# Performance work log

Measured on AMD Instinct MI355X. Metric: run time of the kernel, lower is better.

The kernel has to match this reference:

```python
import jax, jax.numpy as jnp
import numpy as np

H = 16          # num_heads
LN_EPS = 1e-5   # torch LayerNorm default


def _ln(x, g, b):
    m = jnp.mean(x, axis=-1, keepdims=True)
    v = jnp.var(x, axis=-1, keepdims=True)
    return (x - m) * jax.lax.rsqrt(v + LN_EPS) * g + b


def _cross_attn(xq, xkv, wq, wk, wv, wp, bp):
    B, N, C = xq.shape
    d = C // H
    scale = d ** -0.5
    q = (xq @ wq).reshape(B, N, H, d).transpose(0, 2, 1, 3)   # bhnd
    k = (xkv @ wk).reshape(B, N, H, d).transpose(0, 2, 1, 3)
    v = (xkv @ wv).reshape(B, N, H, d).transpose(0, 2, 1, 3)
    attn = jax.nn.softmax(jnp.einsum('bhnd,bhmd->bhnm', q, k) * scale, axis=-1)
    out = jnp.einsum('bhnm,bhmd->bhnd', attn, v).transpose(0, 2, 1, 3).reshape(B, N, C)
    return out @ wp + bp


def setup_inputs() -> dict:
    key = jax.random.key(0)
    ks = jax.random.split(key, 16)
    B, N, C, Hid = 8, 1024, 1024, 4096
    s = 0.02
    inp = {
        'x_1': jax.random.normal(ks[0], (B, N, C), jnp.float32),
        'x_2': jax.random.normal(ks[1], (B, N, C), jnp.float32),
        'x_3': jax.random.normal(ks[2], (B, N, C), jnp.float32),
        'ln11_g': jnp.ones((C,), jnp.float32), 'ln11_b': jnp.zeros((C,), jnp.float32),
        'ln12_g': jnp.ones((C,), jnp.float32), 'ln12_b': jnp.zeros((C,), jnp.float32),
        'ln21_g': jnp.ones((C,), jnp.float32), 'ln21_b': jnp.zeros((C,), jnp.float32),
        'ln23_g': jnp.ones((C,), jnp.float32), 'ln23_b': jnp.zeros((C,), jnp.float32),
        'ln2_g': jnp.ones((C,), jnp.float32), 'ln2_b': jnp.zeros((C,), jnp.float32),
        'a1_wq': s * jax.random.normal(ks[3], (C, C), jnp.float32),
        'a1_wk': s * jax.random.normal(ks[4], (C, C), jnp.float32),
        'a1_wv': s * jax.random.normal(ks[5], (C, C), jnp.float32),
        'a1_wp': s * jax.random.normal(ks[6], (C, C), jnp.float32),
        'a1_bp': jnp.zeros((C,), jnp.float32),
        'a2_wq': s * jax.random.normal(ks[7], (C, C), jnp.float32),
        'a2_wk': s * jax.random.normal(ks[8], (C, C), jnp.float32),
        'a2_wv': s * jax.random.normal(ks[9], (C, C), jnp.float32),
        'a2_wp': s * jax.random.normal(ks[10], (C, C), jnp.float32),
        'a2_bp': jnp.zeros((C,), jnp.float32),
        'fc1_w': s * jax.random.normal(ks[11], (C, Hid), jnp.float32),
        'fc1_b': jnp.zeros((Hid,), jnp.float32),
        'fc2_w': s * jax.random.normal(ks[12], (Hid, C), jnp.float32),
        'fc2_b': jnp.zeros((C,), jnp.float32),
    }
    return inp


def reference(x_1, x_2, x_3,
              ln11_g, ln11_b, ln12_g, ln12_b, ln21_g, ln21_b, ln23_g, ln23_b,
              ln2_g, ln2_b,
              a1_wq, a1_wk, a1_wv, a1_wp, a1_bp,
              a2_wq, a2_wk, a2_wv, a2_wp, a2_bp,
              fc1_w, fc1_b, fc2_w, fc2_b):
    # dual cross-attention branches + residual (drop_path/dropout are identity at p=0)
    br1 = _cross_attn(_ln(x_1, ln11_g, ln11_b), _ln(x_2, ln12_g, ln12_b),
                      a1_wq, a1_wk, a1_wv, a1_wp, a1_bp)
    br2 = _cross_attn(_ln(x_1, ln21_g, ln21_b), _ln(x_3, ln23_g, ln23_b),
                      a2_wq, a2_wk, a2_wv, a2_wp, a2_bp)
    x = x_1 + br1 + br2
    # MLP block
    h = jax.nn.gelu(_ln(x, ln2_g, ln2_b) @ fc1_w + fc1_b, approximate=False)
    x = x + (h @ fc2_w + fc2_b)
    return x
```

## Files before the change

### kernel.cpp

```cpp
#include <hip/hip_runtime.h>
#include <hip/hip_bf16.h>
#include <cstdint>

typedef unsigned short u16;
typedef __bf16 v8bf __attribute__((ext_vector_type(8)));
typedef short v4s __attribute__((ext_vector_type(4)));
typedef float v4f __attribute__((ext_vector_type(4)));

__device__ __forceinline__ u16 f2bf(float f) {
  union { float f; uint32_t u; } v; v.f = f;
  return (u16)((v.u + 0x7fffu + ((v.u >> 16) & 1u)) >> 16);
}
__device__ __forceinline__ float bf2f(u16 u) {
  union { uint32_t u; float f; } v; v.u = ((uint32_t)u) << 16; return v.f;
}
__device__ __forceinline__ float ex2(float x) {
  float r; asm("v_exp_f32 %0, %1" : "=v"(r) : "v"(x)); return r;
}

#define GLL16(gsrc, ldst) \
  __builtin_amdgcn_global_load_lds((__attribute__((address_space(1))) void*)(gsrc), \
      (__attribute__((address_space(3))) void*)(ldst), 16, 0, 0)

#define TILE_MAP(blk, bm, bn) \
  int bm = ((blk) & 7) * 8 + (((blk) >> 3) & 7); \
  int bn = (blk) >> 6;

__device__ __forceinline__ void gemm_core(
    const u16* __restrict__ A, const u16* __restrict__ Bt, int K,
    char* la, char* lb, int bm, int bn, int tid, v4f acc[4][4])
{
  int wv = tid >> 6, lane = tid & 63, quad = lane >> 4, lc = lane & 15;
  int wm = wv & 1, wn = wv >> 1;
  for (int kt = 0; kt < K; kt += 64) {
    __syncthreads();
    #pragma unroll
    for (int c0 = 0; c0 < 4; ++c0) {
      int chunk = wv*4 + c0;
      int off = chunk*1024 + lane*16;
      int row = off >> 7;
      int sc  = (off >> 4) & 7;
      int lg  = sc ^ (row & 7);
      GLL16(A  + (size_t)(bm*128 + row) * K + kt + lg*8, la + chunk*1024);
      GLL16(Bt + (size_t)(bn*128 + row) * K + kt + lg*8, lb + chunk*1024);
    }
    __syncthreads();
    #pragma unroll
    for (int kc = 0; kc < 2; ++kc) {
      v8bf af[4], bfr[4];
      #pragma unroll
      for (int r = 0; r < 4; ++r) {
        int row = wm*64 + r*16 + lc;
        int sc = (kc*4 + quad) ^ (row & 7);
        af[r] = *(const v8bf*)(la + row*128 + sc*16);
      }
      #pragma unroll
      for (int c = 0; c < 4; ++c) {
        int row = wn*64 + c*16 + lc;
        int sc = (kc*4 + quad) ^ (row & 7);
        bfr[c] = *(const v8bf*)(lb + row*128 + sc*16);
      }
      #pragma unroll
      for (int r = 0; r < 4; ++r)
        #pragma unroll
        for (int c = 0; c < 4; ++c)
          acc[r][c] = __builtin_amdgcn_mfma_f32_16x16x32_bf16(af[r], bfr[c], acc[r][c], 0, 0, 0);
    }
  }
}

__device__ __forceinline__ void lds_put16(char* lds_, int row, int col, u16 v) {
  *(u16*)(lds_ + row*256 + (((col >> 4) ^ (row & 7)) << 5) + (col & 15)*2) = v;
}
__device__ __forceinline__ void sweep128(const char* lds_, u16* gout, size_t ldc, int tid) {
  int sub = tid >> 4, j = tid & 15;
  #pragma unroll
  for (int p = 0; p < 8; ++p) {
    int row = p*16 + sub;
    uint4 d = *(const uint4*)(lds_ + row*256 + ((((j >> 1) ^ (row & 7)) << 5) + ((j & 1) << 4)));
    *(uint4*)(gout + (size_t)row*ldc + j*8) = d;
  }
}

struct TDesc { const float* W; u16* WT; int K, N, tstart; };

__device__ __forceinline__ void do_transpose(const TDesc& D, int loc, int tid, float* sh) {
  const float* W = D.W;
  u16* WT = D.WT;
  int K = D.K, N = D.N;
  int tiles_n = N >> 5;
  int bn = loc % tiles_n, bk = loc / tiles_n;
  int tx = tid & 31, ty = tid >> 5;
  #pragma unroll
  for (int j = 0; j < 4; ++j)
    sh[(ty + j*8)*33 + tx] = W[(size_t)(bk*32 + ty + j*8) * N + bn*32 + tx];
  __syncthreads();
  #pragma unroll
  for (int j = 0; j < 4; ++j)
    WT[(size_t)(bn*32 + ty + j*8) * K + bk*32 + tx] = f2bf(sh[tx*33 + ty + j*8]);
}

__device__ __forceinline__ void ln_f32_row(const float* x, const float* g, const float* b,
                                           u16* out, int row, int tid, float* red)
{
  float4 v = ((const float4*)(x + (size_t)row * 1024))[tid];
  float s = v.x + v.y + v.z + v.w;
  float ss = v.x*v.x + v.y*v.y + v.z*v.z + v.w*v.w;
  for (int d = 1; d < 64; d <<= 1) { s += __shfl_xor(s, d); ss += __shfl_xor(ss, d); }
  int wv = tid >> 6, lane = tid & 63;
  if (lane == 0) { red[wv] = s; red[4 + wv] = ss; }
  __syncthreads();
  s  = red[0] + red[1] + red[2] + red[3];
  ss = red[4] + red[5] + red[6] + red[7];
  float mean = s * (1.f/1024.f);
  float var  = ss * (1.f/1024.f) - mean*mean;
  float rs = rsqrtf(var + 1e-5f);
  float4 gv = ((const float4*)g)[tid];
  float4 bv = ((const float4*)b)[tid];
  ushort4 o;
  o.x = f2bf((v.x-mean)*rs*gv.x + bv.x);
  o.y = f2bf((v.y-mean)*rs*gv.y + bv.y);
  o.z = f2bf((v.z-mean)*rs*gv.z + bv.z);
  o.w = f2bf((v.w-mean)*rs*gv.w + bv.w);
  ((ushort4*)out)[(size_t)row*256 + tid] = o;
}

__device__ __forceinline__ void ln_f32_row2(const float* x,
    const float* g1, const float* b1, const float* g2, const float* b2,
    u16* o1, u16* o2, int row, int tid, float* red)
{
  float4 v = ((const float4*)(x + (size_t)row * 1024))[tid];
  float s = v.x + v.y + v.z + v.w;
  float ss = v.x*v.x + v.y*v.y + v.z*v.z + v.w*v.w;
  for (int d = 1; d < 64; d <<= 1) { s += __shfl_xor(s, d); ss += __shfl_xor(ss, d); }
  int wv = tid >> 6, lane = tid & 63;
  if (lane == 0) { red[wv] = s; red[4 + wv] = ss; }
  __syncthreads();
  s  = red[0] + red[1] + red[2] + red[3];
  ss = red[4] + red[5] + red[6] + red[7];
  float mean = s * (1.f/1024.f);
  float var  = ss * (1.f/1024.f) - mean*mean;
  float rs = rsqrtf(var + 1e-5f);
  float4 xn;
  xn.x = (v.x-mean)*rs; xn.y = (v.y-mean)*rs; xn.z = (v.z-mean)*rs; xn.w = (v.w-mean)*rs;
  {
    float4 gv = ((const float4*)g1)[tid];
    float4 bv = ((const float4*)b1)[tid];
    ushort4 o;
    o.x = f2bf(xn.x*gv.x + bv.x); o.y = f2bf(xn.y*gv.y + bv.y);
    o.z = f2bf(xn.z*gv.z + bv.z); o.w = f2bf(xn.w*gv.w + bv.w);
    ((ushort4*)o1)[(size_t)row*256 + tid] = o;
  }
  {
    float4 gv = ((const float4*)g2)[tid];
    float4 bv = ((const float4*)b2)[tid];
    ushort4 o;
    o.x = f2bf(xn.x*gv.x + bv.x); o.y = f2bf(xn.y*gv.y + bv.y);
    o.z = f2bf(xn.z*gv.z + bv.z); o.w = f2bf(xn.w*gv.w + bv.w);
    ((ushort4*)o2)[(size_t)row*256 + tid] = o;
  }
}

struct PrepAll {
  TDesc d[10];
  const float *x1, *g11, *b11, *g21, *b21;
  const float *x2, *g12, *b12;
  const float *x3, *g23, *b23;
  u16 *xq1, *xq2, *xkv1, *xkv2;
  int ts;
};
__global__ __launch_bounds__(256) void prep_all_kernel(PrepAll P)
{
  __shared__ float sh[32*33];
  int tid = threadIdx.x;
  int bi = blockIdx.x;
  if (bi < P.ts) {
    int idx = 0;
    #pragma unroll
    for (int i = 1; i < 10; ++i) if (bi >= P.d[i].tstart) idx = i;
    do_transpose(P.d[idx], bi - P.d[idx].tstart, tid, sh);
  } else {
    int lid = bi - P.ts;
    if (lid < 8192)
      ln_f32_row2(P.x1, P.g11, P.b11, P.g21, P.b21, P.xq1, P.xq2, lid, tid, sh);
    else if (lid < 16384)
      ln_f32_row(P.x2, P.g12, P.b12, P.xkv1, lid - 8192, tid, sh);
    else
      ln_f32_row(P.x3, P.g23, P.b23, P.xkv2, lid - 16384, tid, sh);
  }
}

__global__ __launch_bounds__(256) void ln_bf16_kernel(
    const u16* __restrict__ x, const float* __restrict__ g, const float* __restrict__ bt,
    u16* __restrict__ out)
{
  int row = blockIdx.x, tid = threadIdx.x;
  ushort4 xr = ((const ushort4*)x)[(size_t)row*256 + tid];
  float4 v;
  v.x = bf2f(xr.x); v.y = bf2f(xr.y); v.z = bf2f(xr.z); v.w = bf2f(xr.w);
  float s = v.x + v.y + v.z + v.w;
  float ss = v.x*v.x + v.y*v.y + v.z*v.z + v.w*v.w;
  for (int d = 1; d < 64; d <<= 1) { s += __shfl_xor(s, d); ss += __shfl_xor(ss, d); }
  __shared__ float red[8];
  int wv = tid >> 6, lane = tid & 63;
  if (lane == 0) { red[wv] = s; red[4 + wv] = ss; }
  __syncthreads();
  s  = red[0] + red[1] + red[2] + red[3];
  ss = red[4] + red[5] + red[6] + red[7];
  float mean = s * (1.f/1024.f);
  float var  = ss * (1.f/1024.f) - mean*mean;
  float rs = rsqrtf(var + 1e-5f);
  float4 gv = ((const float4*)g)[tid];
  float4 bv = ((const float4*)bt)[tid];
  ushort4 o;
  o.x = f2bf((v.x-mean)*rs*gv.x + bv.x);
  o.y = f2bf((v.y-mean)*rs*gv.y + bv.y);
  o.z = f2bf((v.z-mean)*rs*gv.z + bv.z);
  o.w = f2bf((v.w-mean)*rs*gv.w + bv.w);
  ((ushort4*)out)[(size_t)row*256 + tid] = o;
}

struct QkvArgs { const u16* A[3]; const u16* Bt[3]; u16* C[3]; };

__device__ __forceinline__ void qkv_body(const QkvArgs& P, int blk, int tid, char* lds_)
{
  int sub = blk >> 9;
  int local = blk & 511;
  TILE_MAP(local, bm, bn)
  int wv = tid >> 6, lane = tid & 63, quad = lane >> 4, lc = lane & 15;
  int wm = wv & 1, wn = wv >> 1;
  v4f acc[4][4] = {};
  gemm_core(P.A[sub], P.Bt[sub], 1024, lds_, lds_ + 16384, bm, bn, tid, acc);
  u16* Cout = P.C[sub];
  __syncthreads();
  if (sub == 2) {
    #pragma unroll
    for (int r = 0; r < 4; ++r) {
      int rl = wm*64 + r*16 + quad*4;
      #pragma unroll
      for (int c = 0; c < 4; ++c) {
        int cl = wn*64 + c*16 + lc;
        #pragma unroll
        for (int i = 0; i < 4; ++i)
          lds_put16(lds_, cl, rl + i, f2bf(acc[r][c][i]));
      }
    }
    __syncthreads();
    sweep128(lds_, Cout + (size_t)(bn*128) * 8192 + bm*128, 8192, tid);
  } else {
    #pragma unroll
    for (int r = 0; r < 4; ++r) {
      int lrow = wm*64 + r*16 + quad*4;
      #pragma unroll
      for (int c = 0; c < 4; ++c) {
        int lcol = wn*64 + c*16 + lc;
        #pragma unroll
        for (int i = 0; i < 4; ++i)
          lds_put16(lds_, lrow + i, lcol, f2bf(acc[r][c][i]));
      }
    }
    __syncthreads();
    sweep128(lds_, Cout + (size_t)(bm*128) * 1024 + bn*128, 1024, tid);
  }
}

__global__ __launch_bounds__(256, 4) void gemm_qkv(QkvArgs P)
{
  __shared__ __align__(16) char lds_[32768];
  qkv_body(P, blockIdx.x, threadIdx.x, lds_);
}

__device__ __forceinline__ void attn_body(
    const u16* __restrict__ Q, const u16* __restrict__ K, const u16* __restrict__ VT,
    u16* __restrict__ O, int bid, int tid, char* lds_)
{
  int qt = bid & 15, h = (bid >> 4) & 15, b = bid >> 8;
  int wv = tid >> 6, lane = tid & 63, quad = lane >> 4, lc = lane & 15;
  char* kt_l = lds_;
  char* vt_l = lds_ + 16384;
  const float cl2 = 0.18033688f;

  v8bf qf[2];
  {
    int qrow = qt*64 + wv*16 + lc;
    const u16* qp = Q + ((size_t)(b*1024 + qrow) * 1024 + h*64 + quad*8);
    qf[0] = *(const v8bf*)qp;
    qf[1] = *(const v8bf*)(qp + 32);
  }

  float m_i = -1e30f, l_i = 0.f;
  v4f oacc[4] = {};

  for (int it = 0; it < 8; ++it) {
    int kvb = it * 128;
    __syncthreads();
    #pragma unroll
    for (int c0 = 0; c0 < 4; ++c0) {
      int ch = wv*4 + c0;
      int off = ch*1024 + lane*16;
      {
        int row = off >> 7, sc = (off >> 4) & 7, lg = sc ^ (row & 7);
        GLL16(K + (size_t)(b*1024 + kvb + row) * 1024 + h*64 + lg*8, kt_l + ch*1024);
      }
      {
        int row = off >> 8, sc = (off >> 4) & 15, lg = sc ^ (row & 15);
        GLL16(VT + (size_t)(h*64 + row) * 8192 + b*1024 + kvb + lg*8, vt_l + ch*1024);
      }
    }
    __syncthreads();

    v4f s[8] = {};
    #pragma unroll
    for (int ct = 0; ct < 8; ++ct) {
      int row = ct*16 + lc;
      #pragma unroll
      for (int kc = 0; kc < 2; ++kc) {
        int sc = (kc*4 + quad) ^ (row & 7);
        v8bf kf = *(const v8bf*)(kt_l + row*128 + sc*16);
        s[ct] = __builtin_amdgcn_mfma_f32_16x16x32_bf16(kf, qf[kc], s[ct], 0, 0, 0);
      }
    }

    #pragma unroll
    for (int ct = 0; ct < 8; ++ct)
      #pragma unroll
      for (int i = 0; i < 4; ++i) s[ct][i] *= cl2;
    float mx = m_i;
    #pragma unroll
    for (int ct = 0; ct < 8; ++ct)
      #pragma unroll
      for (int i = 0; i < 4; ++i) mx = fmaxf(mx, s[ct][i]);
    mx = fmaxf(mx, __shfl_xor(mx, 16));
    mx = fmaxf(mx, __shfl_xor(mx, 32));
    float alpha = ex2(m_i - mx);
    float rs = 0.f;
    #pragma unroll
    for (int ct = 0; ct < 8; ++ct)
      #pragma unroll
      for (int i = 0; i < 4; ++i) {
        float p = ex2(s[ct][i] - mx);
        s[ct][i] = p;
        rs += p;
      }
    rs += __shfl_xor(rs, 16);
    rs += __shfl_xor(rs, 32);
    l_i = l_i * alpha + rs;
    m_i = mx;
    #pragma unroll
    for (int dt = 0; dt < 4; ++dt)
      #pragma unroll
      for (int i = 0; i < 4; ++i) oacc[dt][i] *= alpha;

    #pragma unroll
    for (int ct = 0; ct < 8; ++ct) {
      v4s pfrag;
      #pragma unroll
      for (int i = 0; i < 4; ++i) pfrag[i] = (short)f2bf(s[ct][i]);
      int lg = ct*2 + (quad >> 1);
      int ho = (quad & 1) * 8;
      #pragma unroll
      for (int dt = 0; dt < 4; ++dt) {
        int rowd = dt*16 + lc;
        int sc = lg ^ (rowd & 15);
        v4s vfrag = *(const v4s*)(vt_l + rowd*256 + sc*16 + ho);
        oacc[dt] = __builtin_amdgcn_mfma_f32_16x16x16bf16_1k(vfrag, pfrag, oacc[dt], 0, 0, 0);
      }
    }
  }

  __syncthreads();
  {
    char* base = kt_l + wv*2048;
    float inv = 1.f / l_i;
    #pragma unroll
    for (int dt = 0; dt < 4; ++dt) {
      ushort4 o;
      o.x = f2bf(oacc[dt][0]*inv); o.y = f2bf(oacc[dt][1]*inv);
      o.z = f2bf(oacc[dt][2]*inv); o.w = f2bf(oacc[dt][3]*inv);
      int lg = dt*2 + (quad >> 1);
      int sc = lg ^ (lc & 7);
      *(ushort4*)(base + lc*128 + sc*16 + (quad & 1)*8) = o;
    }
  }
  __syncthreads();
  {
    char* base = kt_l + wv*2048;
    #pragma unroll
    for (int rep = 0; rep < 2; ++rep) {
      int qr = rep*8 + (lane >> 3);
      int ch = lane & 7;
      int sc = ch ^ (qr & 7);
      uint4 d = *(const uint4*)(base + qr*128 + sc*16);
      *(uint4*)(O + (size_t)(b*1024 + qt*64 + wv*16 + qr) * 1024 + h*64 + ch*8) = d;
    }
  }
}

__global__ __launch_bounds__(256, 4) void attn_kernel(
    const u16* __restrict__ Q, const u16* __restrict__ K, const u16* __restrict__ VT,
    u16* __restrict__ O)
{
  __shared__ __align__(16) char lds_[32768];
  attn_body(Q, K, VT, O, blockIdx.x, threadIdx.x, lds_);
}

__global__ __launch_bounds__(256, 4) void attn_qkv_kernel(
    const u16* __restrict__ Q, const u16* __restrict__ K, const u16* __restrict__ VT,
    u16* __restrict__ O, QkvArgs G)
{
  __shared__ __align__(16) char lds_[32768];
  int tid = threadIdx.x;
  if ((int)blockIdx.x < 2048)
    attn_body(Q, K, VT, O, blockIdx.x, tid, lds_);
  else
    qkv_body(G, blockIdx.x - 2048, tid, lds_);
}

__global__ __launch_bounds__(256, 4) void attn_proj_kernel(
    const u16* __restrict__ Q, const u16* __restrict__ K, const u16* __restrict__ VT,
    u16* __restrict__ O,
    const u16* __restrict__ GA, const u16* __restrict__ GBt,
    const float* __restrict__ Gbias, u16* __restrict__ GC)
{
  __shared__ __align__(16) char lds_[32768];
  int tid = threadIdx.x;
  if ((int)blockIdx.x < 2048) {
    attn_body(Q, K, VT, O, blockIdx.x, tid, lds_);
  } else {
    int local = blockIdx.x - 2048;
    TILE_MAP(local, bm, bn)
    int wv = tid >> 6, lane = tid & 63, quad = lane >> 4, lc = lane & 15;
    int wm = wv & 1, wn = wv >> 1;
    v4f acc[4][4] = {};
    gemm_core(GA, GBt, 1024, lds_, lds_ + 16384, bm, bn, tid, acc);
    __syncthreads();
    #pragma unroll
    for (int r = 0; r < 4; ++r) {
      int lrow = wm*64 + r*16 + quad*4;
      #pragma unroll
      for (int c = 0; c < 4; ++c) {
        int lcol = wn*64 + c*16 + lc;
        float bv = Gbias[bn*128 + lcol];
        #pragma unroll
        for (int i = 0; i < 4; ++i)
          lds_put16(lds_, lrow + i, lcol, f2bf(acc[r][c][i] + bv));
      }
    }
    __syncthreads();
    sweep128(lds_, GC + (size_t)(bm*128) * 1024 + bn*128, 1024, tid);
  }
}

__global__ __launch_bounds__(256, 4) void gemm_projadd(
    const u16* __restrict__ A, const u16* __restrict__ Bt,
    const float* __restrict__ bias, const float* __restrict__ x1,
    const u16* __restrict__ o1b, u16* __restrict__ xsum)
{
  TILE_MAP((int)blockIdx.x, bm, bn)
  int tid = threadIdx.x, wv = tid >> 6, lane = tid & 63, quad = lane >> 4, lc = lane & 15;
  int wm = wv & 1, wn = wv >> 1;
  __shared__ __align__(16) char lds_[32768];
  v4f acc[4][4] = {};
  gemm_core(A, Bt, 1024, lds_, lds_ + 16384, bm, bn, tid, acc);
  __syncthreads();
  #pragma unroll
  for (int r = 0; r < 4; ++r) {
    int lrow = wm*64 + r*16 + quad*4;
    int grow = bm*128 + lrow;
    #pragma unroll
    for (int c = 0; c < 4; ++c) {
      int lcol = wn*64 + c*16 + lc;
      int gcol = bn*128 + lcol;
      float bv = bias[gcol];
      #pragma unroll
      for (int i = 0; i < 4; ++i) {
        size_t idx = (size_t)(grow + i) * 1024 + gcol;
        lds_put16(lds_, lrow + i, lcol, f2bf(acc[r][c][i] + bv + x1[idx] + bf2f(o1b[idx])));
      }
    }
  }
  __syncthreads();
  sweep128(lds_, xsum + (size_t)(bm*128) * 1024 + bn*128, 1024, tid);
}

__global__ __launch_bounds__(256, 2) void gemm_fc1(
    const u16* __restrict__ A, const u16* __restrict__ Bt,
    const float* __restrict__ bias, u16* __restrict__ C)
{
  int bm = blockIdx.x >> 5, bn = blockIdx.x & 31;
  int tid = threadIdx.x, wv = tid >> 6, lane = tid & 63, quad = lane >> 4, lc = lane & 15;
  int wm = wv & 1, wn = wv >> 1;
  __shared__ __align__(16) char lds_[32768];
  v4f acc[4][4] = {};
  gemm_core(A, Bt, 1024, lds_, lds_ + 16384, bm, bn, tid, acc);
  __syncthreads();
  #pragma unroll
  for (int r = 0; r < 4; ++r) {
    int lrow = wm*64 + r*16 + quad*4;
    #pragma unroll
    for (int c = 0; c < 4; ++c) {
      int lcol = wn*64 + c*16 + lc;
      float bv = bias[bn*128 + lcol];
      #pragma unroll
      for (int i = 0; i < 4; ++i) {
        float v = acc[r][c][i] + bv;
        float u2 = fminf(2.3023840f * (v + 0.044715f * v * v * v), 115.f);
        float t = ex2(u2);
        lds_put16(lds_, lrow + i, lcol, f2bf(v * t / (t + 1.f)));
      }
    }
  }
  __syncthreads();
  sweep128(lds_, C + (size_t)(bm*128) * 4096 + bn*128, 4096, tid);
}

__global__ __launch_bounds__(256, 3) void gemm_fc2(
    const u16* __restrict__ A, const u16* __restrict__ Bt,
    const float* __restrict__ bias, const u16* __restrict__ r1,
    float* __restrict__ C)
{
  TILE_MAP((int)blockIdx.x, bm, bn)
  int tid = threadIdx.x, wv = tid >> 6, lane = tid & 63, quad = lane >> 4, lc = lane & 15;
  int wm = wv & 1, wn = wv >> 1;
  __shared__ __align__(16) char lds_[32768];
  v4f acc[4][4] = {};
  gemm_core(A, Bt, 4096, lds_, lds_ + 16384, bm, bn, tid, acc);
  #pragma unroll
  for (int r = 0; r < 4; ++r) {
    int grow = bm*128 + wm*64 + r*16 + quad*4;
    #pragma unroll
    for (int c = 0; c < 4; ++c) {
      int gcol = bn*128 + wn*64 + c*16 + lc;
      float bv = bias[gcol];
      #pragma unroll
      for (int i = 0; i < 4; ++i) {
        size_t idx = (size_t)(grow + i) * 1024 + gcol;
        C[idx] = acc[r][c][i] + bv + bf2f(r1[idx]);
      }
    }
  }
}

extern "C" void kernel_launch(void* const* d_in, const int* in_sizes, int n_in,
                              void* d_out, int out_size, void* d_ws, size_t ws_size,
                              hipStream_t stream)
{
  const float* x1    = (const float*)d_in[0];
  const float* x2    = (const float*)d_in[1];
  const float* x3    = (const float*)d_in[2];
  const float* ln11g = (const float*)d_in[3];
  const float* ln11b = (const float*)d_in[4];
  const float* ln12g = (const float*)d_in[5];
  const float* ln12b = (const float*)d_in[6];
  const float* ln21g = (const float*)d_in[7];
  const float* ln21b = (const float*)d_in[8];
  const float* ln23g = (const float*)d_in[9];
  const float* ln23b = (const float*)d_in[10];
  const float* ln2g  = (const float*)d_in[11];
  const float* ln2b  = (const float*)d_in[12];
  const float* a1wq  = (const float*)d_in[13];
  const float* a1wk  = (const float*)d_in[14];
  const float* a1wv  = (const float*)d_in[15];
  const float* a1wp  = (const float*)d_in[16];
  const float* a1bp  = (const float*)d_in[17];
  const float* a2wq  = (const float*)d_in[18];
  const float* a2wk  = (const float*)d_in[19];
  const float* a2wv  = (const float*)d_in[20];
  const float* a2wp  = (const float*)d_in[21];
  const float* a2bp  = (const float*)d_in[22];
  const float* fc1w  = (const float*)d_in[23];
  const float* fc1b  = (const float*)d_in[24];
  const float* fc2w  = (const float*)d_in[25];
  const float* fc2b  = (const float*)d_in[26];

  char* ws = (char*)d_ws;
  const size_t MB = (size_t)1 << 20;
  u16* wtq1 = (u16*)(ws + 0*MB);  u16* wtk1 = (u16*)(ws + 2*MB);
  u16* wtv1 = (u16*)(ws + 4*MB);  u16* wtp1 = (u16*)(ws + 6*MB);
  u16* wtq2 = (u16*)(ws + 8*MB);  u16* wtk2 = (u16*)(ws + 10*MB);
  u16* wtv2 = (u16*)(ws + 12*MB); u16* wtp2 = (u16*)(ws + 14*MB);
  u16* wtf1 = (u16*)(ws + 16*MB); u16* wtf2 = (u16*)(ws + 24*MB);
  u16* xq1  = (u16*)(ws + 32*MB); u16* xkv1 = (u16*)(ws + 48*MB);
  u16* xq2  = (u16*)(ws + 64*MB); u16* xkv2 = (u16*)(ws + 80*MB);
  u16* Qb   = (u16*)(ws + 96*MB); u16* Kb   = (u16*)(ws + 112*MB);
  u16* VTb  = (u16*)(ws + 128*MB);
  u16* O1   = (u16*)(ws + 32*MB);
  u16* o1b  = (u16*)(ws + 64*MB);
  u16* xsum = (u16*)(ws + 112*MB);
  u16* ln2o = (u16*)(ws + 32*MB);
  u16* hbuf = (u16*)(ws + 48*MB);

  bool fused23 = (ws_size >= (size_t)176 * MB);
  u16 *Q2, *K2, *VT2, *O2;
  if (fused23) {
    Q2  = (u16*)(ws + 48*MB);
    K2  = (u16*)(ws + 144*MB);
    VT2 = (u16*)(ws + 160*MB);
    O2  = (u16*)(ws + 96*MB);
  } else {
    Q2 = Qb; K2 = Kb; VT2 = VTb;
    O2  = (u16*)(ws + 48*MB);
  }

  dim3 blk(256);

  PrepAll pa;
  {
    const float* Ws[10]  = {a1wq, a1wk, a1wv, a1wp, a2wq, a2wk, a2wv, a2wp, fc1w, fc2w};
    u16* WTs[10]         = {wtq1, wtk1, wtv1, wtp1, wtq2, wtk2, wtv2, wtp2, wtf1, wtf2};
    int Kd[10] = {1024,1024,1024,1024,1024,1024,1024,1024,1024,4096};
    int Nd[10] = {1024,1024,1024,1024,1024,1024,1024,1024,4096,1024};
    int ts = 0;
    for (int i = 0; i < 10; ++i) {
      pa.d[i] = {Ws[i], WTs[i], Kd[i], Nd[i], ts};
      ts += (Kd[i]/32) * (Nd[i]/32);
    }
    pa.ts = ts;
  }
  pa.x1 = x1; pa.g11 = ln11g; pa.b11 = ln11b; pa.g21 = ln21g; pa.b21 = ln21b;
  pa.x2 = x2; pa.g12 = ln12g; pa.b12 = ln12b;
  pa.x3 = x3; pa.g23 = ln23g; pa.b23 = ln23b;
  pa.xq1 = xq1; pa.xq2 = xq2; pa.xkv1 = xkv1; pa.xkv2 = xkv2;
  prep_all_kernel<<<pa.ts + 24576, blk, 0, stream>>>(pa);

  QkvArgs g1;
  g1.A[0]=xq1;  g1.Bt[0]=wtq1; g1.C[0]=Qb;
  g1.A[1]=xkv1; g1.Bt[1]=wtk1; g1.C[1]=Kb;
  g1.A[2]=xkv1; g1.Bt[2]=wtv1; g1.C[2]=VTb;
  gemm_qkv<<<1536, blk, 0, stream>>>(g1);

  QkvArgs g2;
  g2.A[0]=xq2;  g2.Bt[0]=wtq2; g2.C[0]=Q2;
  g2.A[1]=xkv2; g2.Bt[1]=wtk2; g2.C[1]=K2;
  g2.A[2]=xkv2; g2.Bt[2]=wtv2; g2.C[2]=VT2;
  if (fused23) {
    attn_qkv_kernel<<<2048 + 1536, blk, 0, stream>>>(Qb, Kb, VTb, O1, g2);
  } else {
    attn_kernel<<<2048, blk, 0, stream>>>(Qb, Kb, VTb, O1);
    gemm_qkv<<<1536, blk, 0, stream>>>(g2);
  }

  attn_proj_kernel<<<2048 + 512, blk, 0, stream>>>(Q2, K2, VT2, O2, O1, wtp1, a1bp, o1b);

  gemm_projadd<<<512, blk, 0, stream>>>(O2, wtp2, a2bp, x1, o1b, xsum);

  ln_bf16_kernel<<<8192, blk, 0, stream>>>(xsum, ln2g, ln2b, ln2o);

  gemm_fc1<<<2048, blk, 0, stream>>>(ln2o, wtf1, fc1b, hbuf);

  gemm_fc2<<<512, blk, 0, stream>>>(hbuf, wtf2, fc2b, xsum, (float*)d_out);
}
```

Before: 693.2 us.

## Fold softmax scale into Q, add lazy rescaling, pack conversions, tune occupancy

The softmax scale (log2e/sqrt(d)) is now folded into the Q projection epilogue, so the attention loop no longer multiplies every score. Online softmax skips rescaling the output accumulator when the new block max stays within a threshold of the running max, and P is converted to bf16 with packed hardware converts. Other changes: the V^T epilogue writes 4-element vectors with a new LDS swizzle, the LN kernel handles four rows per block, and the attention kernels raise launch-bound occupancy to 5. The lazy rescale lets exponents reach up to 2^8 before renormalising, and the higher occupancy target may force register spills.

```diff
diff --git a/kernel.cpp b/kernel.cpp
--- a/kernel.cpp
+++ b/kernel.cpp
@@ -25,6 +25,8 @@
 #define TILE_MAP(blk, bm, bn) \
   int bm = ((blk) & 7) * 8 + (((blk) >> 3) & 7); \
   int bn = (blk) >> 6;
+
+#define QSCALE 0.18033688f
 
 __device__ __forceinline__ void gemm_core(
     const u16* __restrict__ A, const u16* __restrict__ Bt, int K,
@@ -194,30 +196,35 @@
     const u16* __restrict__ x, const float* __restrict__ g, const float* __restrict__ bt,
     u16* __restrict__ out)
 {
-  int row = blockIdx.x, tid = threadIdx.x;
-  ushort4 xr = ((const ushort4*)x)[(size_t)row*256 + tid];
-  float4 v;
-  v.x = bf2f(xr.x); v.y = bf2f(xr.y); v.z = bf2f(xr.z); v.w = bf2f(xr.w);
-  float s = v.x + v.y + v.z + v.w;
-  float ss = v.x*v.x + v.y*v.y + v.z*v.z + v.w*v.w;
-  for (int d = 1; d < 64; d <<= 1) { s += __shfl_xor(s, d); ss += __shfl_xor(ss, d); }
+  int tid = threadIdx.x;
   __shared__ float red[8];
-  int wv = tid >> 6, lane = tid & 63;
-  if (lane == 0) { red[wv] = s; red[4 + wv] = ss; }
-  __syncthreads();
-  s  = red[0] + red[1] + red[2] + red[3];
-  ss = red[4] + red[5] + red[6] + red[7];
-  float mean = s * (1.f/1024.f);
-  float var  = ss * (1.f/1024.f) - mean*mean;
-  float rs = rsqrtf(var + 1e-5f);
   float4 gv = ((const float4*)g)[tid];
   float4 bv = ((const float4*)bt)[tid];
-  ushort4 o;
-  o.x = f2bf((v.x-mean)*rs*gv.x + bv.x);
-  o.y = f2bf((v.y-mean)*rs*gv.y + bv.y);
-  o.z = f2bf((v.z-mean)*rs*gv.z + bv.z);
-  o.w = f2bf((v.w-mean)*rs*gv.w + bv.w);
-  ((ushort4*)out)[(size_t)row*256 + tid] = o;
+  #pragma unroll
+  for (int rr = 0; rr < 4; ++rr) {
+    int row = blockIdx.x*4 + rr;
+    ushort4 xr = ((const ushort4*)x)[(size_t)row*256 + tid];
+    float4 v;
+    v.x = bf2f(xr.x); v.y = bf2f(xr.y); v.z = bf2f(xr.z); v.w = bf2f(xr.w);
+    float s = v.x + v.y + v.z + v.w;
+    float ss = v.x*v.x + v.y*v.y + v.z*v.z + v.w*v.w;
+    for (int d = 1; d < 64; d <<= 1) { s += __shfl_xor(s, d); ss += __shfl_xor(ss, d); }
+    int wv = tid >> 6, lane = tid & 63;
+    if (lane == 0) { red[wv] = s; red[4 + wv] = ss; }
+    __syncthreads();
+    s  = red[0] + red[1] + red[2] + red[3];
+    ss = red[4] + red[5] + red[6] + red[7];
+    float mean = s * (1.f/1024.f);
+    float var  = ss * (1.f/1024.f) - mean*mean;
+    float rs = rsqrtf(var + 1e-5f);
+    ushort4 o;
+    o.x = f2bf((v.x-mean)*rs*gv.x + bv.x);
+    o.y = f2bf((v.y-mean)*rs*gv.y + bv.y);
+    o.z = f2bf((v.z-mean)*rs*gv.z + bv.z);
+    o.w = f2bf((v.w-mean)*rs*gv.w + bv.w);
+    ((ushort4*)out)[(size_t)row*256 + tid] = o;
+    __syncthreads();
+  }
 }
 
 struct QkvArgs { const u16* A[3]; const u16* Bt[3]; u16* C[3]; };
@@ -240,14 +247,17 @@
       #pragma unroll
       for (int c = 0; c < 4; ++c) {
         int cl = wn*64 + c*16 + lc;
+        v4s o;
         #pragma unroll
-        for (int i = 0; i < 4; ++i)
-          lds_put16(lds_, cl, rl + i, f2bf(acc[r][c][i]));
+        for (int i = 0; i < 4; ++i) o[i] = (short)f2bf(acc[r][c][i]);
+        int chunk = ((rl >> 4) ^ (cl & 7)) << 5;
+        *(v4s*)(lds_ + cl*256 + chunk + (rl & 15)*2) = o;
       }
     }
     __syncthreads();
     sweep128(lds_, Cout + (size_t)(bn*128) * 8192 + bm*128, 8192, tid);
   } else {
+    float scl = (sub == 0) ? QSCALE : 1.f;
     #pragma unroll
     for (int r = 0; r < 4; ++r) {
       int lrow = wm*64 + r*16 + quad*4;
@@ -256,7 +266,7 @@
         int lcol = wn*64 + c*16 + lc;
         #pragma unroll
         for (int i = 0; i < 4; ++i)
-          lds_put16(lds_, lrow + i, lcol, f2bf(acc[r][c][i]));
+          lds_put16(lds_, lrow + i, lcol, f2bf(acc[r][c][i] * scl));
       }
     }
     __syncthreads();
@@ -278,7 +288,6 @@
   int wv = tid >> 6, lane = tid & 63, quad = lane >> 4, lc = lane & 15;
   char* kt_l = lds_;
   char* vt_l = lds_ + 16384;
-  const float cl2 = 0.18033688f;
 
   v8bf qf[2];
   {
@@ -321,18 +330,17 @@
       }
     }
 
+    float pmax = s[0][0];
     #pragma unroll
     for (int ct = 0; ct < 8; ++ct)
       #pragma unroll
-      for (int i = 0; i < 4; ++i) s[ct][i] *= cl2;
-    float mx = m_i;
-    #pragma unroll
-    for (int ct = 0; ct < 8; ++ct)
-      #pragma unroll
-      for (int i = 0; i < 4; ++i) mx = fmaxf(mx, s[ct][i]);
-    mx = fmaxf(mx, __shfl_xor(mx, 16));
-    mx = fmaxf(mx, __shfl_xor(mx, 32));
-    float alpha = ex2(m_i - mx);
+      for (int i = 0; i < 4; ++i) pmax = fmaxf(pmax, s[ct][i]);
+    pmax = fmaxf(pmax, __shfl_xor(pmax, 16));
+    pmax = fmaxf(pmax, __shfl_xor(pmax, 32));
+
+    bool stable = __all(pmax <= m_i + 8.f);
+    float mx = stable ? m_i : fmaxf(m_i, pmax);
+
     float rs = 0.f;
     #pragma unroll
     for (int ct = 0; ct < 8; ++ct)
@@ -344,18 +352,24 @@
       }
     rs += __shfl_xor(rs, 16);
     rs += __shfl_xor(rs, 32);
-    l_i = l_i * alpha + rs;
-    m_i = mx;
-    #pragma unroll
-    for (int dt = 0; dt < 4; ++dt)
-      #pragma unroll
-      for (int i = 0; i < 4; ++i) oacc[dt][i] *= alpha;
+    if (stable) {
+      l_i += rs;
+    } else {
+      float alpha = ex2(m_i - mx);
+      l_i = l_i * alpha + rs;
+      #pragma unroll
+      for (int dt = 0; dt < 4; ++dt)
+        #pragma unroll
+        for (int i = 0; i < 4; ++i) oacc[dt][i] *= alpha;
+      m_i = mx;
+    }
 
     #pragma unroll
     for (int ct = 0; ct < 8; ++ct) {
-      v4s pfrag;
-      #pragma unroll
-      for (int i = 0; i < 4; ++i) pfrag[i] = (short)f2bf(s[ct][i]);
+      union { uint32_t u[2]; v4s p; } pk;
+      asm("v_cvt_pk_bf16_f32 %0, %1, %2" : "=v"(pk.u[0]) : "v"(s[ct][0]), "v"(s[ct][1]));
+      asm("v_cvt_pk_bf16_f32 %0, %1, %2" : "=v"(pk.u[1]) : "v"(s[ct][2]), "v"(s[ct][3]));
+      v4s pfrag = pk.p;
       int lg = ct*2 + (quad >> 1);
       int ho = (quad & 1) * 8;
       #pragma unroll
@@ -396,7 +410,7 @@
   }
 }
 
-__global__ __launch_bounds__(256, 4) void attn_kernel(
+__global__ __launch_bounds__(256, 5) void attn_kernel(
     const u16* __restrict__ Q, const u16* __restrict__ K, const u16* __restrict__ VT,
     u16* __restrict__ O)
 {
@@ -404,7 +418,7 @@
   attn_body(Q, K, VT, O, blockIdx.x, threadIdx.x, lds_);
 }
 
-__global__ __launch_bounds__(256, 4) void attn_qkv_kernel(
+__global__ __launch_bounds__(256, 5) void attn_qkv_kernel(
     const u16* __restrict__ Q, const u16* __restrict__ K, const u16* __restrict__ VT,
     u16* __restrict__ O, QkvArgs G)
 {
@@ -416,7 +430,7 @@
     qkv_body(G, blockIdx.x - 2048, tid, lds_);
 }
 
-__global__ __launch_bounds__(256, 4) void attn_proj_kernel(
+__global__ __launch_bounds__(256, 5) void attn_proj_kernel(
     const u16* __restrict__ Q, const u16* __restrict__ K, const u16* __restrict__ VT,
     u16* __restrict__ O,
     const u16* __restrict__ GA, const u16* __restrict__ GBt,
@@ -644,7 +658,7 @@
 
   gemm_projadd<<<512, blk, 0, stream>>>(O2, wtp2, a2bp, x1, o1b, xsum);
 
-  ln_bf16_kernel<<<8192, blk, 0, stream>>>(xsum, ln2g, ln2b, ln2o);
+  ln_bf16_kernel<<<2048, blk, 0, stream>>>(xsum, ln2g, ln2b, ln2o);
 
   gemm_fc1<<<2048, blk, 0, stream>>>(ln2o, wtf1, fc1b, hbuf);
 
```

Measured after the change: 805.6 us. 1.16x slower.
